# Kernel optimization log

Measured on AMD Instinct MI355X. Metric: run time of the kernel, lower is better.

The kernel has to match this reference:

```python
import jax, jax.numpy as jnp
import numpy as np


def setup_inputs() -> dict:
    key = jax.random.key(0)
    ks = jax.random.split(key, 7)
    N, H, W, C, O, K, WD, NW = 16, 64, 64, 512, 512, 3, 512, 14
    return {
        "x": jax.random.normal(ks[0], (N, H, W, C), jnp.float32),
        "dlatents": jax.random.normal(ks[1], (N, NW, WD), jnp.float32),
        "style_w": jax.random.normal(ks[2], (WD, C), jnp.float32),
        "style_b": jnp.ones((C,), jnp.float32),          # bias_init=1 in LinearLayer
        "weight": jax.random.normal(ks[3], (K, K, C, O), jnp.float32),
        "bias": jax.random.normal(ks[4], (O,), jnp.float32) * 0.1,
        "noise_strength": jax.random.normal(ks[5], (), jnp.float32) * 0.1,
        "noise": jax.random.normal(ks[6], (N, H, W, 1), jnp.float32),
        "layer_idx": 7,
    }


def reference(x, dlatents, style_w, style_b, weight, bias, noise_strength, noise, layer_idx):
    N, H, W, C = x.shape
    K = weight.shape[0]
    w_dim = dlatents.shape[-1]
    # Style linear with equalized learning rate (he_std = 1/sqrt(in), lr_multiplier = 1)
    dl = dlatents[:, layer_idx]                               # [N, w_dim]
    s = dl @ (style_w * (1.0 / np.sqrt(w_dim))) + style_b     # [N, C] per-sample styles
    # Equalized-lr conv weight
    w = weight * (1.0 / np.sqrt(K * K * C))                   # [K, K, C, O]
    # Demodulation coeffs d[n,o] = rsqrt(sum_{k,k,i} (w*s)^2 + eps), computed
    # without materializing the per-sample [N,K,K,C,O] modulated weights.
    d = jax.lax.rsqrt(jnp.einsum('hwio,ni->no', jnp.square(w), jnp.square(s)) + 1e-8)  # [N, O]
    # Non-fused modulated conv: scale inputs, shared-weight conv, scale outputs.
    y = jax.lax.conv_general_dilated(
        x * s[:, None, None, :], w,
        window_strides=(1, 1), padding='SAME',
        dimension_numbers=('NHWC', 'HWIO', 'NHWC'))           # [N, H, W, O]
    y = y * d[:, None, None, :]
    # Noise injection + bias + activation (leaky_relu with gain sqrt(2))
    y = y + noise * noise_strength
    y = y + bias
    return jax.nn.leaky_relu(y, 0.2) * np.sqrt(2.0)
```

## Files before the change

### kernel.cpp

```cpp
#include <hip/hip_runtime.h>
#include <hip/hip_bf16.h>

typedef __attribute__((ext_vector_type(8))) short bf16x8;
typedef __attribute__((ext_vector_type(4))) float f32x4;
typedef __attribute__((ext_vector_type(8))) short shortx8;

#define WBT_OFF_B 71368704ull
#define S_OFF_B   76087296ull
#define D_OFF_B   76120064ull
#define W2_OFF_B  76152832ull

__device__ __forceinline__ void gload16(const void* g, void* l) {
  __builtin_amdgcn_global_load_lds((const __attribute__((address_space(1))) void*)g,
                                   (__attribute__((address_space(3))) void*)l, 16, 0, 0);
}

__global__ void style_kernel(const float* __restrict__ dlat, const float* __restrict__ sw,
                             const float* __restrict__ sb, const int* __restrict__ lidx,
                             float* __restrict__ s) {
  int gid = blockIdx.x * 256 + threadIdx.x;
  int n = gid >> 9, c = gid & 511;
  const float* dl = dlat + (n * 14 + lidx[0]) * 512;
  float acc = 0.f;
#pragma unroll 4
  for (int k = 0; k < 512; ++k) acc = fmaf(dl[k], sw[k * 512 + c], acc);
  s[gid] = acc * 0.044194173824159216f + sb[c];
}

__global__ void w2_kernel(const float* __restrict__ weight, float* __restrict__ w2) {
  int gid = blockIdx.x * 256 + threadIdx.x;
  int i = gid >> 9, o = gid & 511;
  float acc = 0.f;
#pragma unroll
  for (int t = 0; t < 9; ++t) { float v = weight[(t * 512 + i) * 512 + o]; acc = fmaf(v, v, acc); }
  w2[gid] = acc;
}

__global__ void dpart_kernel(const float* __restrict__ w2, const float* __restrict__ s,
                             float* __restrict__ dpre) {
  int b = blockIdx.x;
  int n = b >> 3, ic = (b >> 1) & 3, oh = b & 1;
  int o = (oh << 8) + threadIdx.x;
  const float* sn = s + (n << 9) + (ic << 7);
  const float* w2p = w2 + ((ic << 7) << 9) + o;
  float acc = 0.f;
#pragma unroll 4
  for (int i = 0; i < 128; ++i) { float sv = sn[i]; acc = fmaf(w2p[i << 9], sv * sv, acc); }
  atomicAdd(&dpre[(n << 9) + o], acc);
}

__global__ void wbt_kernel(const float* __restrict__ weight, __hip_bfloat16* __restrict__ wbT) {
  __shared__ float tile[64][65];
  int b = blockIdx.x;
  int t = b >> 6; int rem = b & 63;
  int i0 = (rem >> 3) << 6, o0 = (rem & 7) << 6;
  int tr = threadIdx.x >> 4;
  int tc = (threadIdx.x & 15) << 2;
#pragma unroll
  for (int rr = 0; rr < 4; ++rr) {
    int il = tr + (rr << 4);
    float4 v = *(const float4*)&weight[((size_t)(t * 512 + i0 + il) << 9) + o0 + tc];
    tile[il][tc] = v.x; tile[il][tc + 1] = v.y; tile[il][tc + 2] = v.z; tile[il][tc + 3] = v.w;
  }
  __syncthreads();
#pragma unroll
  for (int rr = 0; rr < 4; ++rr) {
    int ol = tr + (rr << 4);
    short4 ov;
#pragma unroll
    for (int j = 0; j < 4; ++j) {
      __hip_bfloat16 h = __float2bfloat16(tile[tc + j][ol] * 0.014731391274719739f);
      ((short*)&ov)[j] = *(short*)&h;
    }
    *(short4*)&wbT[((size_t)(t * 512 + o0 + ol) << 9) + i0 + tc] = ov;
  }
}

__global__ void xpad_kernel(const float* __restrict__ x, const float* __restrict__ s,
                            __hip_bfloat16* __restrict__ xsp) {
  int gid = blockIdx.x * 256 + threadIdx.x;
  int c8 = gid & 63;
  int pos = gid >> 6;
  int wp = pos % 66; int t1 = pos / 66; int hp = t1 % 66; int n = t1 / 66;
  shortx8 ov;
  if ((unsigned)(hp - 1) < 64u && (unsigned)(wp - 1) < 64u) {
    const float* xp = &x[((((n << 6) + (hp - 1)) << 6) + (wp - 1)) * 512 + (c8 << 3)];
    const float* sp = &s[(n << 9) + (c8 << 3)];
    float4 a0 = *(const float4*)xp, a1 = *(const float4*)(xp + 4);
    float4 s0 = *(const float4*)sp, s1 = *(const float4*)(sp + 4);
    float r[8] = {a0.x * s0.x, a0.y * s0.y, a0.z * s0.z, a0.w * s0.w,
                  a1.x * s1.x, a1.y * s1.y, a1.z * s1.z, a1.w * s1.w};
#pragma unroll
    for (int j = 0; j < 8; ++j) { __hip_bfloat16 h = __float2bfloat16(r[j]); ov[j] = *(short*)&h; }
  } else {
#pragma unroll
    for (int j = 0; j < 8; ++j) ov[j] = 0;
  }
  *(shortx8*)&xsp[(size_t)pos * 512 + (c8 << 3)] = ov;
}

__global__ void conv_kernel(const __hip_bfloat16* __restrict__ xsp,
                            const __hip_bfloat16* __restrict__ wbT,
                            const float* __restrict__ dpre,
                            const float* __restrict__ bias,
                            const float* __restrict__ noise,
                            const float* __restrict__ nstr,
                            float* __restrict__ out) {
  __shared__ short Ald[128 * 32];
  __shared__ short Bld[128 * 32];

  int bid = blockIdx.x;
  bid = (bid & 7) * 256 + (bid >> 3);
  int mTile = bid >> 2, nTile = bid & 3;

  int tid = threadIdx.x;
  int lane = tid & 63, wv = tid >> 6;
  int wm = wv >> 1, wn = wv & 1;

  int m_base = mTile << 7;
  int n_img = m_base >> 12;
  int h_b = (m_base & 4095) >> 6;
  int oB = nTile << 7;

  int rlow = (wv << 4) + (lane >> 2);
  int seg = (lane & 3) << 3;

  int xb0 = ((n_img * 66 + h_b) * 66 + rlow) * 512 + seg;
  int xb1 = ((n_img * 66 + h_b + 1) * 66 + rlow) * 512 + seg;
  int bb0 = (oB + rlow) * 512 + seg;
  int bb1 = (oB + 64 + rlow) * 512 + seg;

  short* la0 = &Ald[wv * 512];
  short* la1 = &Ald[(4 + wv) * 512];
  short* lb0 = &Bld[wv * 512];
  short* lb1 = &Bld[(4 + wv) * 512];

  int arow = (wm << 6) + (lane & 15);
  int brow = (wn << 6) + (lane & 15);
  int koff = (lane >> 4) << 3;

  f32x4 acc[4][4];
#pragma unroll
  for (int f = 0; f < 4; ++f)
#pragma unroll
    for (int g = 0; g < 4; ++g) acc[f][g] = {0.f, 0.f, 0.f, 0.f};

#pragma unroll 1
  for (int tap = 0; tap < 9; ++tap) {
    int toff = ((tap / 3) * 66 + (tap % 3)) * 512;
    const __hip_bfloat16* ga0 = xsp + xb0 + toff;
    const __hip_bfloat16* ga1 = xsp + xb1 + toff;
    const __hip_bfloat16* gb0 = wbT + tap * 262144 + bb0;
    const __hip_bfloat16* gb1 = wbT + tap * 262144 + bb1;
#pragma unroll 1
    for (int kb = 0; kb < 16; ++kb) {
      __syncthreads();
      gload16(ga0, la0); gload16(ga1, la1);
      gload16(gb0, lb0); gload16(gb1, lb1);
      __syncthreads();
      ga0 += 32; ga1 += 32; gb0 += 32; gb1 += 32;
      bf16x8 af[4], bfr[4];
#pragma unroll
      for (int f = 0; f < 4; ++f) af[f] = *(const bf16x8*)&Ald[(arow + (f << 4)) * 32 + koff];
#pragma unroll
      for (int g = 0; g < 4; ++g) bfr[g] = *(const bf16x8*)&Bld[(brow + (g << 4)) * 32 + koff];
#pragma unroll
      for (int f = 0; f < 4; ++f)
#pragma unroll
        for (int g = 0; g < 4; ++g)
          acc[f][g] = __builtin_amdgcn_mfma_f32_16x16x32_bf16(af[f], bfr[g], acc[f][g], 0, 0, 0);
    }
  }

  float ns = nstr[0];
  int ocol = oB + (wn << 6) + (lane & 15);
  float dv[4], bv[4];
#pragma unroll
  for (int g = 0; g < 4; ++g) {
    dv[g] = rsqrtf(dpre[(n_img << 9) + ocol + (g << 4)] * (1.0f / 4608.0f) + 1e-8f);
    bv[g] = bias[ocol + (g << 4)];
  }
  int mrow0 = m_base + (wm << 6) + ((lane >> 4) << 2);
#pragma unroll
  for (int f = 0; f < 4; ++f) {
#pragma unroll
    for (int j = 0; j < 4; ++j) {
      int m = mrow0 + (f << 4) + j;
      float nz = noise[m] * ns;
      float* op = out + (size_t)m * 512 + ocol;
#pragma unroll
      for (int g = 0; g < 4; ++g) {
        float v = fmaf(acc[f][g][j], dv[g], nz + bv[g]);
        v = (v > 0.f ? v : 0.2f * v) * 1.4142135623730951f;
        op[g << 4] = v;
      }
    }
  }
}

extern "C" void kernel_launch(void* const* d_in, const int* in_sizes, int n_in,
                              void* d_out, int out_size, void* d_ws, size_t ws_size,
                              hipStream_t stream) {
  const float* x     = (const float*)d_in[0];
  const float* dlat  = (const float*)d_in[1];
  const float* sw    = (const float*)d_in[2];
  const float* sb    = (const float*)d_in[3];
  const float* wt    = (const float*)d_in[4];
  const float* bias  = (const float*)d_in[5];
  const float* nstr  = (const float*)d_in[6];
  const float* noise = (const float*)d_in[7];
  const int*   lidx  = (const int*)d_in[8];
  float* out = (float*)d_out;

  char* ws = (char*)d_ws;
  __hip_bfloat16* xsp = (__hip_bfloat16*)ws;
  __hip_bfloat16* wbT = (__hip_bfloat16*)(ws + WBT_OFF_B);
  float* sbuf = (float*)(ws + S_OFF_B);
  float* dpre = (float*)(ws + D_OFF_B);
  float* w2   = (float*)(ws + W2_OFF_B);

  hipMemsetAsync(dpre, 0, 16 * 512 * sizeof(float), stream);
  style_kernel<<<32, 256, 0, stream>>>(dlat, sw, sb, lidx, sbuf);
  w2_kernel<<<1024, 256, 0, stream>>>(wt, w2);
  dpart_kernel<<<128, 256, 0, stream>>>(w2, sbuf, dpre);
  wbt_kernel<<<576, 256, 0, stream>>>(wt, wbT);
  xpad_kernel<<<17424, 256, 0, stream>>>(x, sbuf, xsp);
  conv_kernel<<<2048, 256, 0, stream>>>(xsp, wbT, dpre, bias, noise, nstr, out);
}
```

Before: 641.2 us.

## Restructure conv GEMM with 256x128 tiles, triple-buffered LDS and swizzle

The implicit-GEMM conv kernel now uses 512-thread blocks with 256x128 output tiles and a K-step of 64. Global-to-LDS loads are triple-buffered and issued two iterations ahead, interleaved with four MFMA phases that use raised wave priority and explicit barriers. An XOR swizzle on the LDS layout avoids bank conflicts. The aim is to hide load latency behind compute and raise data reuse per block, at the cost of 144KB of dynamic LDS per block and fragile hand scheduling with manual waitcnt.

Measured after the change: 623.7 us. 2.7% less time.

```diff
diff --git a/kernel.cpp b/kernel.cpp
--- a/kernel.cpp
+++ b/kernel.cpp
@@ -14,6 +14,9 @@
   __builtin_amdgcn_global_load_lds((const __attribute__((address_space(1))) void*)g,
                                    (__attribute__((address_space(3))) void*)l, 16, 0, 0);
 }
+
+#define BAR() do { __builtin_amdgcn_s_barrier(); __builtin_amdgcn_sched_barrier(0); } while (0)
+
 
 __global__ void style_kernel(const float* __restrict__ dlat, const float* __restrict__ sw,
                              const float* __restrict__ sb, const int* __restrict__ lidx,
@@ -99,45 +102,62 @@
   *(shortx8*)&xsp[(size_t)pos * 512 + (c8 << 3)] = ov;
 }
 
-__global__ void conv_kernel(const __hip_bfloat16* __restrict__ xsp,
-                            const __hip_bfloat16* __restrict__ wbT,
-                            const float* __restrict__ dpre,
-                            const float* __restrict__ bias,
-                            const float* __restrict__ noise,
-                            const float* __restrict__ nstr,
-                            float* __restrict__ out) {
-  __shared__ short Ald[128 * 32];
-  __shared__ short Bld[128 * 32];
+
+__global__ __launch_bounds__(512, 2) void conv_kernel(
+    const __hip_bfloat16* __restrict__ xsp,
+    const __hip_bfloat16* __restrict__ wbT,
+    const float* __restrict__ dpre,
+    const float* __restrict__ bias,
+    const float* __restrict__ noise,
+    const float* __restrict__ nstr,
+    float* __restrict__ out) {
+  extern __shared__ short lds[];
 
   int bid = blockIdx.x;
-  bid = (bid & 7) * 256 + (bid >> 3);
+  bid = (bid & 7) * 128 + (bid >> 3);
   int mTile = bid >> 2, nTile = bid & 3;
-
-  int tid = threadIdx.x;
-  int lane = tid & 63, wv = tid >> 6;
+  int mBase = mTile << 8;
+  int n_img = mBase >> 12;
+  int oB = nTile << 7;
+
+  int tid = threadIdx.x, lane = tid & 63, wv = tid >> 6;
   int wm = wv >> 1, wn = wv & 1;
 
-  int m_base = mTile << 7;
-  int n_img = m_base >> 12;
-  int h_b = (m_base & 4095) >> 6;
-  int oB = nTile << 7;
-
-  int rlow = (wv << 4) + (lane >> 2);
-  int seg = (lane & 3) << 3;
-
-  int xb0 = ((n_img * 66 + h_b) * 66 + rlow) * 512 + seg;
-  int xb1 = ((n_img * 66 + h_b + 1) * 66 + rlow) * 512 + seg;
-  int bb0 = (oB + rlow) * 512 + seg;
-  int bb1 = (oB + 64 + rlow) * 512 + seg;
-
-  short* la0 = &Ald[wv * 512];
-  short* la1 = &Ald[(4 + wv) * 512];
-  short* lb0 = &Bld[wv * 512];
-  short* lb1 = &Bld[(4 + wv) * 512];
-
-  int arow = (wm << 6) + (lane & 15);
-  int brow = (wn << 6) + (lane & 15);
-  int koff = (lane >> 4) << 3;
+  int r0 = tid >> 3, r1 = (tid + 512) >> 3;
+  int cg0 = (tid & 7) ^ (r0 & 7);
+  int cg1 = (tid & 7) ^ (r1 & 7);
+
+  int m00 = mBase + r0, m01 = mBase + r1;
+  int m10 = mBase + 128 + r0, m11 = mBase + 128 + r1;
+  int a00 = ((n_img * 66 + ((m00 >> 6) & 63)) * 66 + (m00 & 63)) * 512 + cg0 * 8;
+  int a01 = ((n_img * 66 + ((m01 >> 6) & 63)) * 66 + (m01 & 63)) * 512 + cg1 * 8;
+  int a10 = ((n_img * 66 + ((m10 >> 6) & 63)) * 66 + (m10 & 63)) * 512 + cg0 * 8;
+  int a11 = ((n_img * 66 + ((m11 >> 6) & 63)) * 66 + (m11 & 63)) * 512 + cg1 * 8;
+  int b0 = (oB + r0) * 512 + cg0 * 8;
+  int b1 = (oB + r1) * 512 + cg1 * 8;
+
+  int dA = wv * 512;
+  int dB = 16384 + wv * 512;
+
+  auto stageB = [&](int bu, int add) {
+    short* base = lds + bu * 24576 + dB;
+    gload16(wbT + b0 + add, base);
+    gload16(wbT + b1 + add, base + 4096);
+  };
+  auto stageA0 = [&](int bu, int add) {
+    short* base = lds + bu * 24576 + dA;
+    gload16(xsp + a00 + add, base);
+    gload16(xsp + a01 + add, base + 4096);
+  };
+  auto stageA1 = [&](int bu, int add) {
+    short* base = lds + bu * 24576 + 8192 + dA;
+    gload16(xsp + a10 + add, base);
+    gload16(xsp + a11 + add, base + 4096);
+  };
+
+  int l15 = lane & 15, l16 = lane >> 4;
+  int arowb = wm * 64 + l15;
+  int browb = wn * 64 + l15;
 
   f32x4 acc[4][4];
 #pragma unroll
@@ -145,54 +165,102 @@
 #pragma unroll
     for (int g = 0; g < 4; ++g) acc[f][g] = {0.f, 0.f, 0.f, 0.f};
 
+  stageB(0, 0); stageA0(0, 0); stageA1(0, 0);
+  stageB(1, 64); stageA0(1, 64); stageA1(1, 64);
+  asm volatile("s_waitcnt vmcnt(6)" ::: "memory");
+  BAR();
+
+  int cur = 0, sb = 2;
 #pragma unroll 1
-  for (int tap = 0; tap < 9; ++tap) {
-    int toff = ((tap / 3) * 66 + (tap % 3)) * 512;
-    const __hip_bfloat16* ga0 = xsp + xb0 + toff;
-    const __hip_bfloat16* ga1 = xsp + xb1 + toff;
-    const __hip_bfloat16* gb0 = wbT + tap * 262144 + bb0;
-    const __hip_bfloat16* gb1 = wbT + tap * 262144 + bb1;
-#pragma unroll 1
-    for (int kb = 0; kb < 16; ++kb) {
-      __syncthreads();
-      gload16(ga0, la0); gload16(ga1, la1);
-      gload16(gb0, lb0); gload16(gb1, lb1);
-      __syncthreads();
-      ga0 += 32; ga1 += 32; gb0 += 32; gb1 += 32;
-      bf16x8 af[4], bfr[4];
-#pragma unroll
-      for (int f = 0; f < 4; ++f) af[f] = *(const bf16x8*)&Ald[(arow + (f << 4)) * 32 + koff];
-#pragma unroll
-      for (int g = 0; g < 4; ++g) bfr[g] = *(const bf16x8*)&Bld[(brow + (g << 4)) * 32 + koff];
-#pragma unroll
-      for (int f = 0; f < 4; ++f)
-#pragma unroll
-        for (int g = 0; g < 4; ++g)
-          acc[f][g] = __builtin_amdgcn_mfma_f32_16x16x32_bf16(af[f], bfr[g], acc[f][g], 0, 0, 0);
-    }
+  for (int t = 0; t < 72; ++t) {
+    short* L = lds + cur * 24576;
+    int u = t + 2;
+    bool doStage = u < 72;
+    int tp = u >> 3, kt = u & 7;
+    int aAdd = ((tp / 3) * 66 + (tp % 3)) * 512 + kt * 64;
+    int bAdd = tp * 262144 + kt * 64;
+
+#define AF(F, KS) (*(const bf16x8*)&L[(arowb + (F)*16) * 64 + ((((KS)*4 + l16) ^ ((arowb + (F)*16) & 7)) << 3)])
+#define BFR(G, KS) (*(const bf16x8*)&L[16384 + (browb + (G)*16) * 64 + ((((KS)*4 + l16) ^ ((browb + (G)*16) & 7)) << 3)])
+#define PHASE_MFMA(F) \
+    acc[F][0] = __builtin_amdgcn_mfma_f32_16x16x32_bf16(a0, b00, acc[F][0], 0, 0, 0); \
+    acc[F][0] = __builtin_amdgcn_mfma_f32_16x16x32_bf16(a1, b01, acc[F][0], 0, 0, 0); \
+    acc[F][1] = __builtin_amdgcn_mfma_f32_16x16x32_bf16(a0, b10, acc[F][1], 0, 0, 0); \
+    acc[F][1] = __builtin_amdgcn_mfma_f32_16x16x32_bf16(a1, b11, acc[F][1], 0, 0, 0); \
+    acc[F][2] = __builtin_amdgcn_mfma_f32_16x16x32_bf16(a0, b20, acc[F][2], 0, 0, 0); \
+    acc[F][2] = __builtin_amdgcn_mfma_f32_16x16x32_bf16(a1, b21, acc[F][2], 0, 0, 0); \
+    acc[F][3] = __builtin_amdgcn_mfma_f32_16x16x32_bf16(a0, b30, acc[F][3], 0, 0, 0); \
+    acc[F][3] = __builtin_amdgcn_mfma_f32_16x16x32_bf16(a1, b31, acc[F][3], 0, 0, 0);
+
+    bf16x8 b00 = BFR(0, 0), b01 = BFR(0, 1), b10 = BFR(1, 0), b11 = BFR(1, 1);
+    bf16x8 b20 = BFR(2, 0), b21 = BFR(2, 1), b30 = BFR(3, 0), b31 = BFR(3, 1);
+    bf16x8 a0 = AF(0, 0), a1 = AF(0, 1);
+    if (doStage) stageB(sb, bAdd);
+    BAR();
+    asm volatile("s_waitcnt lgkmcnt(0)" ::: "memory");
+    __builtin_amdgcn_sched_barrier(0);
+    __builtin_amdgcn_s_setprio(1);
+    PHASE_MFMA(0)
+    __builtin_amdgcn_s_setprio(0);
+    BAR();
+
+    a0 = AF(1, 0); a1 = AF(1, 1);
+    if (doStage) stageA0(sb, aAdd);
+    BAR();
+    asm volatile("s_waitcnt lgkmcnt(0)" ::: "memory");
+    __builtin_amdgcn_sched_barrier(0);
+    __builtin_amdgcn_s_setprio(1);
+    PHASE_MFMA(1)
+    __builtin_amdgcn_s_setprio(0);
+    BAR();
+
+    a0 = AF(2, 0); a1 = AF(2, 1);
+    if (doStage) stageA1(sb, aAdd);
+    BAR();
+    asm volatile("s_waitcnt lgkmcnt(0)" ::: "memory");
+    __builtin_amdgcn_sched_barrier(0);
+    __builtin_amdgcn_s_setprio(1);
+    PHASE_MFMA(2)
+    __builtin_amdgcn_s_setprio(0);
+    BAR();
+
+    a0 = AF(3, 0); a1 = AF(3, 1);
+    if (t < 70) { asm volatile("s_waitcnt vmcnt(6)" ::: "memory"); }
+    else        { asm volatile("s_waitcnt vmcnt(0)" ::: "memory"); }
+    BAR();
+    asm volatile("s_waitcnt lgkmcnt(0)" ::: "memory");
+    __builtin_amdgcn_sched_barrier(0);
+    __builtin_amdgcn_s_setprio(1);
+    PHASE_MFMA(3)
+    __builtin_amdgcn_s_setprio(0);
+    BAR();
+
+    cur = (cur == 2) ? 0 : cur + 1;
+    sb = (sb == 2) ? 0 : sb + 1;
   }
 
   float ns = nstr[0];
-  int ocol = oB + (wn << 6) + (lane & 15);
+  int ocol = oB + wn * 64 + l15;
   float dv[4], bv[4];
 #pragma unroll
   for (int g = 0; g < 4; ++g) {
-    dv[g] = rsqrtf(dpre[(n_img << 9) + ocol + (g << 4)] * (1.0f / 4608.0f) + 1e-8f);
-    bv[g] = bias[ocol + (g << 4)];
-  }
-  int mrow0 = m_base + (wm << 6) + ((lane >> 4) << 2);
+    int o = ocol + g * 16;
+    dv[g] = rsqrtf(dpre[(n_img << 9) + o] * (1.0f / 4608.0f) + 1e-8f);
+    bv[g] = bias[o];
+  }
+  int mrow0 = mBase + wm * 64 + (l16 << 2);
 #pragma unroll
   for (int f = 0; f < 4; ++f) {
 #pragma unroll
     for (int j = 0; j < 4; ++j) {
-      int m = mrow0 + (f << 4) + j;
+      int m = mrow0 + f * 16 + j;
       float nz = noise[m] * ns;
       float* op = out + (size_t)m * 512 + ocol;
 #pragma unroll
       for (int g = 0; g < 4; ++g) {
         float v = fmaf(acc[f][g][j], dv[g], nz + bv[g]);
         v = (v > 0.f ? v : 0.2f * v) * 1.4142135623730951f;
-        op[g << 4] = v;
+        op[g * 16] = v;
       }
     }
   }
@@ -219,11 +287,14 @@
   float* dpre = (float*)(ws + D_OFF_B);
   float* w2   = (float*)(ws + W2_OFF_B);
 
+  hipFuncSetAttribute((const void*)conv_kernel,
+                      hipFuncAttributeMaxDynamicSharedMemorySize, 147456);
+
   hipMemsetAsync(dpre, 0, 16 * 512 * sizeof(float), stream);
   style_kernel<<<32, 256, 0, stream>>>(dlat, sw, sb, lidx, sbuf);
   w2_kernel<<<1024, 256, 0, stream>>>(wt, w2);
   dpart_kernel<<<128, 256, 0, stream>>>(w2, sbuf, dpre);
   wbt_kernel<<<576, 256, 0, stream>>>(wt, wbT);
   xpad_kernel<<<17424, 256, 0, stream>>>(x, sbuf, xsp);
-  conv_kernel<<<2048, 256, 0, stream>>>(xsp, wbT, dpre, bias, noise, nstr, out);
-}
+  conv_kernel<<<1024, 512, 147456, stream>>>(xsp, wbT, dpre, bias, noise, nstr, out);
+}
```
